# Kernel optimization log

Hardware: AMD Instinct MI355X
Metric: run time of the kernel (lower is better)

The kernel has to match this reference:

```python
import jax, jax.numpy as jnp
import numpy as np

B, C, N = 16, 128, 16384


def setup_inputs() -> dict:
    key = jax.random.key(0)
    k1, k2, k3, k4, k5 = jax.random.split(key, 5)
    scale = 1.0 / np.sqrt(C)
    return {
        "feature": jax.random.normal(k1, (B, C, N), dtype=jnp.float32),
        "position": jax.random.normal(k2, (B, C, N), dtype=jnp.float32),
        "Wq": jax.random.normal(k3, (C, C), dtype=jnp.float32) * scale,
        "Wk": jax.random.normal(k4, (C, C), dtype=jnp.float32) * scale,
        "Wv": jax.random.normal(k5, (C, C), dtype=jnp.float32) * scale,
    }


def reference(feature, position, Wq, Wk, Wv):
    # 1x1 Conv1d == channel-mixing matmul: (B,C,N) x (Cout,Cin) -> (B,Cout,N)
    q = jnp.einsum("oc,bcn->bon", Wq, position)  # (B,C,N)
    k = jnp.einsum("oc,bcn->bon", Wk, position)  # (B,C,N)
    v = jnp.einsum("oc,bcn->bon", Wv, feature)   # (B,C,N)

    # torch: matmul((B,N,C,1),(B,N,1,C)).sum(dim=-2) == (sum_c q) * k
    # -> energy[b,j,n] = sq[b,n] * k[b,j,n], avoiding the (B,N,C,C) tensor.
    sq = jnp.sum(q, axis=1, keepdims=True)       # (B,1,N)
    energy = sq * k                              # (B,C,N)

    # normalize over the channel axis (torch's dim=-1 on (B,N,C) layout)
    energy = energy / (1e-9 + jnp.sum(energy, axis=1, keepdims=True))

    # softmax over channel axis (torch: Softmax(dim=1) on permuted (B,C,N))
    attention = jax.nn.softmax(energy, axis=1)   # (B,C,N)

    return attention * v + feature               # (B,C,N)
```

## Files before the change

### kernel.cpp

```cpp
#include <hip/hip_runtime.h>

#define B_ 16
#define C_ 128
#define N_ 16384
#define TN 32

typedef __attribute__((ext_vector_type(8))) short short8;
typedef __attribute__((ext_vector_type(4))) float f32x4;

__device__ inline unsigned short bf16_rn(float x) {
  unsigned u = __float_as_uint(x);
  unsigned r = u + 0x7FFFu + ((u >> 16) & 1u);
  return (unsigned short)(r >> 16);
}

__device__ inline unsigned cvt_pk_bf16(float a, float b) {
  unsigned r;
  asm("v_cvt_pk_bf16_f32 %0, %1, %2" : "=v"(r) : "v"(a), "v"(b));
  return r;
}

__global__ __launch_bounds__(256) void prep_kernel(
    const float* __restrict__ Wq, const float* __restrict__ Wk, const float* __restrict__ Wv,
    float* __restrict__ wqsum,
    unsigned short* __restrict__ WkHi, unsigned short* __restrict__ WkLo,
    unsigned short* __restrict__ WvHi) {
  int idx = blockIdx.x * 256 + threadIdx.x;
  {
    float x = Wk[idx];
    unsigned short h = bf16_rn(x);
    WkHi[idx] = h;
    WkLo[idx] = bf16_rn(x - __uint_as_float(((unsigned)h) << 16));
  }
  WvHi[idx] = bf16_rn(Wv[idx]);
  if (blockIdx.x == 0 && threadIdx.x < C_) {
    int i = threadIdx.x;
    float s = 0.f;
#pragma unroll 8
    for (int o = 0; o < C_; ++o) s += Wq[o * C_ + i];
    wqsum[i] = s;
  }
}

__global__ __launch_bounds__(256, 6) void csa_mfma_kernel(
    const float* __restrict__ feature, const float* __restrict__ position,
    const float* __restrict__ wqsum,
    const unsigned short* __restrict__ WkHi, const unsigned short* __restrict__ WkLo,
    const unsigned short* __restrict__ WvHi,
    float* __restrict__ out) {
  __shared__ unsigned short posHi[TN * 128];
  __shared__ unsigned short posLo[TN * 128];
  __shared__ unsigned short featHi[TN * 128];
  __shared__ float red0[4][TN];
  __shared__ float red1[4][TN];
  __shared__ float red2[4][TN];
  __shared__ float red3[4][TN];

  const int tid = threadIdx.x;
  const int lane = tid & 63;
  const int w = tid >> 6;
  const int m = lane & 15;
  const int q = lane >> 4;
  const int b = blockIdx.x >> 9;
  const int n0 = (blockIdx.x & 511) * TN;

  const float* pos_g = position + (size_t)b * C_ * N_ + n0;
  const float* feat_g = feature + (size_t)b * C_ * N_ + n0;

  {
    const int g = tid >> 3;
    const int n4 = (tid & 7) * 4;
    f32x4 sqa = (f32x4){0.f, 0.f, 0.f, 0.f};
#pragma unroll
    for (int it = 0; it < 2; ++it) {
      int i = 64 * it + 2 * g;
      float4 p0 = *(const float4*)(pos_g + (size_t)i * N_ + n4);
      float4 p1 = *(const float4*)(pos_g + (size_t)(i + 1) * N_ + n4);
      float4 f0 = *(const float4*)(feat_g + (size_t)i * N_ + n4);
      float4 f1 = *(const float4*)(feat_g + (size_t)(i + 1) * N_ + n4);
      float2 wq2 = *(const float2*)(wqsum + i);
      const float* P0 = (const float*)&p0;
      const float* P1 = (const float*)&p1;
      const float* F0 = (const float*)&f0;
      const float* F1 = (const float*)&f1;
      int c8 = (i >> 3) * 8;
      int ioff = i & 7;
#pragma unroll
      for (int d = 0; d < 4; ++d) {
        int n = n4 + d;
        int fn8 = ((n & 15) ^ ((n >> 2) & 7)) * 8;
        int hw = n * 128 + (c8 ^ fn8) + ioff;
        float x0 = P0[d], x1 = P1[d];
        unsigned hu = cvt_pk_bf16(x0, x1);
        *(unsigned*)(posHi + hw) = hu;
        float l0 = x0 - __uint_as_float(hu << 16);
        float l1 = x1 - __uint_as_float(hu & 0xFFFF0000u);
        *(unsigned*)(posLo + hw) = cvt_pk_bf16(l0, l1);
        *(unsigned*)(featHi + hw) = cvt_pk_bf16(F0[d], F1[d]);
        sqa[d] = fmaf(wq2.x, x0, fmaf(wq2.y, x1, sqa[d]));
      }
    }
#pragma unroll
    for (int d = 0; d < 4; ++d) {
      float s = sqa[d];
      s += __shfl_xor(s, 8, 64);
      s += __shfl_xor(s, 16, 64);
      s += __shfl_xor(s, 32, 64);
      sqa[d] = s;
    }
    if (lane < 8) {
      *(float4*)&red0[w][lane * 4] =
          make_float4(sqa[0], sqa[1], sqa[2], sqa[3]);
    }
  }
  __syncthreads();

  int rb[2], f8[2];
#pragma unroll
  for (int nt = 0; nt < 2; ++nt) {
    int n = nt * 16 + m;
    rb[nt] = n * 128;
    f8[nt] = ((n & 15) ^ ((n >> 2) & 7)) * 8;
  }

  f32x4 acck[2][2];
#pragma unroll
  for (int jt = 0; jt < 2; ++jt)
#pragma unroll
    for (int nt = 0; nt < 2; ++nt) acck[jt][nt] = (f32x4){0.f, 0.f, 0.f, 0.f};

#pragma unroll
  for (int jt = 0; jt < 2; ++jt) {
    const int arow = (32 * w + 16 * jt + m) * 128 + q * 8;
    short8 ah[4], al[4];
#pragma unroll
    for (int kk = 0; kk < 4; ++kk) {
      ah[kk] = *(const short8*)(WkHi + arow + kk * 32);
      al[kk] = *(const short8*)(WkLo + arow + kk * 32);
    }
#pragma unroll
    for (int kk = 0; kk < 4; ++kk) {
      int co = (kk * 4 + q) * 8;
      short8 bh0 = *(const short8*)(posHi + rb[0] + (co ^ f8[0]));
      short8 bl0 = *(const short8*)(posLo + rb[0] + (co ^ f8[0]));
      short8 bh1 = *(const short8*)(posHi + rb[1] + (co ^ f8[1]));
      short8 bl1 = *(const short8*)(posLo + rb[1] + (co ^ f8[1]));
      acck[jt][0] = __builtin_amdgcn_mfma_f32_16x16x32_bf16(ah[kk], bh0, acck[jt][0], 0, 0, 0);
      acck[jt][1] = __builtin_amdgcn_mfma_f32_16x16x32_bf16(ah[kk], bh1, acck[jt][1], 0, 0, 0);
      acck[jt][0] = __builtin_amdgcn_mfma_f32_16x16x32_bf16(ah[kk], bl0, acck[jt][0], 0, 0, 0);
      acck[jt][1] = __builtin_amdgcn_mfma_f32_16x16x32_bf16(ah[kk], bl1, acck[jt][1], 0, 0, 0);
      acck[jt][0] = __builtin_amdgcn_mfma_f32_16x16x32_bf16(al[kk], bh0, acck[jt][0], 0, 0, 0);
      acck[jt][1] = __builtin_amdgcn_mfma_f32_16x16x32_bf16(al[kk], bh1, acck[jt][1], 0, 0, 0);
    }
  }

#pragma unroll
  for (int nt = 0; nt < 2; ++nt) {
    float s = 0.f;
#pragma unroll
    for (int jt = 0; jt < 2; ++jt)
      s += acck[jt][nt][0] + acck[jt][nt][1] + acck[jt][nt][2] + acck[jt][nt][3];
    s += __shfl_xor(s, 16, 64);
    s += __shfl_xor(s, 32, 64);
    if (q == 0) red1[w][nt * 16 + m] = s;
  }

  f32x4 accv[2][2];
#pragma unroll
  for (int jt = 0; jt < 2; ++jt)
#pragma unroll
    for (int nt = 0; nt < 2; ++nt) accv[jt][nt] = (f32x4){0.f, 0.f, 0.f, 0.f};

#pragma unroll
  for (int jt = 0; jt < 2; ++jt) {
    const int arow = (32 * w + 16 * jt + m) * 128 + q * 8;
    short8 ah[4];
#pragma unroll
    for (int kk = 0; kk < 4; ++kk) ah[kk] = *(const short8*)(WvHi + arow + kk * 32);
#pragma unroll
    for (int kk = 0; kk < 4; ++kk) {
      int co = (kk * 4 + q) * 8;
      short8 bh0 = *(const short8*)(featHi + rb[0] + (co ^ f8[0]));
      short8 bh1 = *(const short8*)(featHi + rb[1] + (co ^ f8[1]));
      accv[jt][0] = __builtin_amdgcn_mfma_f32_16x16x32_bf16(ah[kk], bh0, accv[jt][0], 0, 0, 0);
      accv[jt][1] = __builtin_amdgcn_mfma_f32_16x16x32_bf16(ah[kk], bh1, accv[jt][1], 0, 0, 0);
    }
  }
  __syncthreads();

  float mw[2], sw[2], attscale[2];
#pragma unroll
  for (int nt = 0; nt < 2; ++nt) {
    int c = nt * 16 + m;
    float ss = red0[0][c] + red0[1][c] + red0[2][c] + red0[3][c];
    float ks = red1[0][c] + red1[1][c] + red1[2][c] + red1[3][c];
    float gl = (ss / (1e-9f + ss * ks)) * 1.44269504f;
    float mx = gl * acck[0][nt][0];
#pragma unroll
    for (int jt = 0; jt < 2; ++jt)
#pragma unroll
      for (int r = 0; r < 4; ++r) {
        float e = gl * acck[jt][nt][r];
        acck[jt][nt][r] = e;
        mx = fmaxf(mx, e);
      }
    mx = fmaxf(mx, __shfl_xor(mx, 16, 64));
    mx = fmaxf(mx, __shfl_xor(mx, 32, 64));
    float s = 0.f;
#pragma unroll
    for (int jt = 0; jt < 2; ++jt)
#pragma unroll
      for (int r = 0; r < 4; ++r) {
        float p = exp2f(acck[jt][nt][r] - mx);
        acck[jt][nt][r] = p;
        s += p;
      }
    s += __shfl_xor(s, 16, 64);
    s += __shfl_xor(s, 32, 64);
    mw[nt] = mx;
    sw[nt] = s;
  }
  if (q == 0) {
#pragma unroll
    for (int nt = 0; nt < 2; ++nt) {
      red2[w][nt * 16 + m] = mw[nt];
      red3[w][nt * 16 + m] = sw[nt];
    }
  }
  __syncthreads();
#pragma unroll
  for (int nt = 0; nt < 2; ++nt) {
    int c = nt * 16 + m;
    float M = red2[0][c];
    M = fmaxf(M, red2[1][c]);
    M = fmaxf(M, red2[2][c]);
    M = fmaxf(M, red2[3][c]);
    float es = red3[0][c] * exp2f(red2[0][c] - M);
    es += red3[1][c] * exp2f(red2[1][c] - M);
    es += red3[2][c] * exp2f(red2[2][c] - M);
    es += red3[3][c] * exp2f(red2[3][c] - M);
    attscale[nt] = exp2f(mw[nt] - M) / es;
  }

  float* outp = out + (size_t)b * C_ * N_ + n0 + m;
  const float* finp = feature + (size_t)b * C_ * N_ + n0 + m;
#pragma unroll
  for (int jt = 0; jt < 2; ++jt) {
    const int jb = 32 * w + 16 * jt + 4 * q;
#pragma unroll
    for (int nt = 0; nt < 2; ++nt) {
      float as = attscale[nt];
      size_t base = (size_t)jb * N_ + nt * 16;
      float fv0 = finp[base];
      float fv1 = finp[base + N_];
      float fv2 = finp[base + (size_t)2 * N_];
      float fv3 = finp[base + (size_t)3 * N_];
      outp[base] = fmaf(acck[jt][nt][0] * as, accv[jt][nt][0], fv0);
      outp[base + N_] = fmaf(acck[jt][nt][1] * as, accv[jt][nt][1], fv1);
      outp[base + (size_t)2 * N_] = fmaf(acck[jt][nt][2] * as, accv[jt][nt][2], fv2);
      outp[base + (size_t)3 * N_] = fmaf(acck[jt][nt][3] * as, accv[jt][nt][3], fv3);
    }
  }
}

extern "C" void kernel_launch(void* const* d_in, const int* in_sizes, int n_in,
                              void* d_out, int out_size, void* d_ws, size_t ws_size,
                              hipStream_t stream) {
  const float* feature = (const float*)d_in[0];
  const float* position = (const float*)d_in[1];
  const float* Wq = (const float*)d_in[2];
  const float* Wk = (const float*)d_in[3];
  const float* Wv = (const float*)d_in[4];
  float* out = (float*)d_out;

  char* ws = (char*)d_ws;
  float* wqsum = (float*)ws;
  unsigned short* WkHi = (unsigned short*)(ws + 512);
  unsigned short* WkLo = (unsigned short*)(ws + 512 + 32768);
  unsigned short* WvHi = (unsigned short*)(ws + 512 + 65536);

  prep_kernel<<<64, 256, 0, stream>>>(Wq, Wk, Wv, wqsum, WkHi, WkLo, WvHi);
  csa_mfma_kernel<<<B_ * (N_ / TN), 256, 0, stream>>>(feature, position, wqsum,
                                                      WkHi, WkLo, WvHi, out);
}
```

Baseline: 399.0 us.

## Process multiple tiles per block with register prefetch and LDS-based residual

Each block now handles four consecutive 32-column tiles, issuing global loads for the next tile into registers while computing the current one. Feature is also split into hi/lo bf16 in LDS so the residual add reconstructs it from shared memory instead of re-reading global memory. This aims to hide load latency and cut redundant DRAM traffic, at the cost of fewer blocks, higher register/LDS use, lower occupancy, and slightly reduced precision of the residual term.

Result: slower. 519.5 us (+30.2%).

```diff
diff --git a/kernel.cpp b/kernel.cpp
--- a/kernel.cpp
+++ b/kernel.cpp
@@ -4,6 +4,7 @@
 #define C_ 128
 #define N_ 16384
 #define TN 32
+#define NT 4
 
 typedef __attribute__((ext_vector_type(8))) short short8;
 typedef __attribute__((ext_vector_type(4))) float f32x4;
@@ -19,6 +20,9 @@
   asm("v_cvt_pk_bf16_f32 %0, %1, %2" : "=v"(r) : "v"(a), "v"(b));
   return r;
 }
+
+__device__ inline float u16hi_f(unsigned u) { return __uint_as_float(u & 0xFFFF0000u); }
+__device__ inline float u16lo_f(unsigned u) { return __uint_as_float(u << 16); }
 
 __global__ __launch_bounds__(256) void prep_kernel(
     const float* __restrict__ Wq, const float* __restrict__ Wk, const float* __restrict__ Wv,
@@ -42,7 +46,7 @@
   }
 }
 
-__global__ __launch_bounds__(256, 6) void csa_mfma_kernel(
+__global__ __launch_bounds__(256, 4) void csa_mfma_kernel(
     const float* __restrict__ feature, const float* __restrict__ position,
     const float* __restrict__ wqsum,
     const unsigned short* __restrict__ WkHi, const unsigned short* __restrict__ WkLo,
@@ -51,6 +55,7 @@
   __shared__ unsigned short posHi[TN * 128];
   __shared__ unsigned short posLo[TN * 128];
   __shared__ unsigned short featHi[TN * 128];
+  __shared__ unsigned short featLo[TN * 128];
   __shared__ float red0[4][TN];
   __shared__ float red1[4][TN];
   __shared__ float red2[4][TN];
@@ -61,28 +66,50 @@
   const int w = tid >> 6;
   const int m = lane & 15;
   const int q = lane >> 4;
-  const int b = blockIdx.x >> 9;
-  const int n0 = (blockIdx.x & 511) * TN;
-
-  const float* pos_g = position + (size_t)b * C_ * N_ + n0;
-  const float* feat_g = feature + (size_t)b * C_ * N_ + n0;
-
-  {
-    const int g = tid >> 3;
-    const int n4 = (tid & 7) * 4;
-    f32x4 sqa = (f32x4){0.f, 0.f, 0.f, 0.f};
+  const int b = blockIdx.x >> 7;
+  const int ncol0 = (blockIdx.x & 127) * (TN * NT);
+
+  const float* pos_g = position + (size_t)b * C_ * N_ + ncol0;
+  const float* feat_g = feature + (size_t)b * C_ * N_ + ncol0;
+
+  const int g = tid >> 3;
+  const int n4 = (tid & 7) * 4;
+  const float2 wq0 = *(const float2*)(wqsum + 2 * g);
+  const float2 wq1 = *(const float2*)(wqsum + 64 + 2 * g);
+
+  int rb[2], f8[2];
+#pragma unroll
+  for (int nt = 0; nt < 2; ++nt) {
+    int n = nt * 16 + m;
+    rb[nt] = n * 128;
+    f8[nt] = ((n & 15) ^ ((n >> 2) & 7)) * 8;
+  }
+
+  float4 P0[2], P1[2], F0[2], F1[2];
+
+  auto issue_loads = [&](int t) {
+    const float* pg = pos_g + t * TN;
+    const float* fg = feat_g + t * TN;
 #pragma unroll
     for (int it = 0; it < 2; ++it) {
       int i = 64 * it + 2 * g;
-      float4 p0 = *(const float4*)(pos_g + (size_t)i * N_ + n4);
-      float4 p1 = *(const float4*)(pos_g + (size_t)(i + 1) * N_ + n4);
-      float4 f0 = *(const float4*)(feat_g + (size_t)i * N_ + n4);
-      float4 f1 = *(const float4*)(feat_g + (size_t)(i + 1) * N_ + n4);
-      float2 wq2 = *(const float2*)(wqsum + i);
-      const float* P0 = (const float*)&p0;
-      const float* P1 = (const float*)&p1;
-      const float* F0 = (const float*)&f0;
-      const float* F1 = (const float*)&f1;
+      P0[it] = *(const float4*)(pg + (size_t)i * N_ + n4);
+      P1[it] = *(const float4*)(pg + (size_t)(i + 1) * N_ + n4);
+      F0[it] = *(const float4*)(fg + (size_t)i * N_ + n4);
+      F1[it] = *(const float4*)(fg + (size_t)(i + 1) * N_ + n4);
+    }
+  };
+
+  auto stage_convert = [&]() {
+    f32x4 sqa = (f32x4){0.f, 0.f, 0.f, 0.f};
+#pragma unroll
+    for (int it = 0; it < 2; ++it) {
+      int i = 64 * it + 2 * g;
+      float2 wq2 = it ? wq1 : wq0;
+      const float* P0p = (const float*)&P0[it];
+      const float* P1p = (const float*)&P1[it];
+      const float* F0p = (const float*)&F0[it];
+      const float* F1p = (const float*)&F1[it];
       int c8 = (i >> 3) * 8;
       int ioff = i & 7;
 #pragma unroll
@@ -90,13 +117,18 @@
         int n = n4 + d;
         int fn8 = ((n & 15) ^ ((n >> 2) & 7)) * 8;
         int hw = n * 128 + (c8 ^ fn8) + ioff;
-        float x0 = P0[d], x1 = P1[d];
+        float x0 = P0p[d], x1 = P1p[d];
         unsigned hu = cvt_pk_bf16(x0, x1);
         *(unsigned*)(posHi + hw) = hu;
-        float l0 = x0 - __uint_as_float(hu << 16);
-        float l1 = x1 - __uint_as_float(hu & 0xFFFF0000u);
+        float l0 = x0 - u16lo_f(hu);
+        float l1 = x1 - u16hi_f(hu);
         *(unsigned*)(posLo + hw) = cvt_pk_bf16(l0, l1);
-        *(unsigned*)(featHi + hw) = cvt_pk_bf16(F0[d], F1[d]);
+        float y0 = F0p[d], y1 = F1p[d];
+        unsigned fu = cvt_pk_bf16(y0, y1);
+        *(unsigned*)(featHi + hw) = fu;
+        float e0 = y0 - u16lo_f(fu);
+        float e1 = y1 - u16hi_f(fu);
+        *(unsigned*)(featLo + hw) = cvt_pk_bf16(e0, e1);
         sqa[d] = fmaf(wq2.x, x0, fmaf(wq2.y, x1, sqa[d]));
       }
     }
@@ -109,156 +141,176 @@
       sqa[d] = s;
     }
     if (lane < 8) {
-      *(float4*)&red0[w][lane * 4] =
-          make_float4(sqa[0], sqa[1], sqa[2], sqa[3]);
-    }
-  }
+      *(float4*)&red0[w][lane * 4] = make_float4(sqa[0], sqa[1], sqa[2], sqa[3]);
+    }
+  };
+
+  issue_loads(0);
+  stage_convert();
   __syncthreads();
 
-  int rb[2], f8[2];
-#pragma unroll
-  for (int nt = 0; nt < 2; ++nt) {
-    int n = nt * 16 + m;
-    rb[nt] = n * 128;
-    f8[nt] = ((n & 15) ^ ((n >> 2) & 7)) * 8;
-  }
-
-  f32x4 acck[2][2];
-#pragma unroll
-  for (int jt = 0; jt < 2; ++jt)
-#pragma unroll
-    for (int nt = 0; nt < 2; ++nt) acck[jt][nt] = (f32x4){0.f, 0.f, 0.f, 0.f};
-
-#pragma unroll
-  for (int jt = 0; jt < 2; ++jt) {
-    const int arow = (32 * w + 16 * jt + m) * 128 + q * 8;
-    short8 ah[4], al[4];
-#pragma unroll
-    for (int kk = 0; kk < 4; ++kk) {
-      ah[kk] = *(const short8*)(WkHi + arow + kk * 32);
-      al[kk] = *(const short8*)(WkLo + arow + kk * 32);
-    }
-#pragma unroll
-    for (int kk = 0; kk < 4; ++kk) {
-      int co = (kk * 4 + q) * 8;
-      short8 bh0 = *(const short8*)(posHi + rb[0] + (co ^ f8[0]));
-      short8 bl0 = *(const short8*)(posLo + rb[0] + (co ^ f8[0]));
-      short8 bh1 = *(const short8*)(posHi + rb[1] + (co ^ f8[1]));
-      short8 bl1 = *(const short8*)(posLo + rb[1] + (co ^ f8[1]));
-      acck[jt][0] = __builtin_amdgcn_mfma_f32_16x16x32_bf16(ah[kk], bh0, acck[jt][0], 0, 0, 0);
-      acck[jt][1] = __builtin_amdgcn_mfma_f32_16x16x32_bf16(ah[kk], bh1, acck[jt][1], 0, 0, 0);
-      acck[jt][0] = __builtin_amdgcn_mfma_f32_16x16x32_bf16(ah[kk], bl0, acck[jt][0], 0, 0, 0);
-      acck[jt][1] = __builtin_amdgcn_mfma_f32_16x16x32_bf16(ah[kk], bl1, acck[jt][1], 0, 0, 0);
-      acck[jt][0] = __builtin_amdgcn_mfma_f32_16x16x32_bf16(al[kk], bh0, acck[jt][0], 0, 0, 0);
-      acck[jt][1] = __builtin_amdgcn_mfma_f32_16x16x32_bf16(al[kk], bh1, acck[jt][1], 0, 0, 0);
-    }
-  }
-
-#pragma unroll
-  for (int nt = 0; nt < 2; ++nt) {
-    float s = 0.f;
+#pragma unroll
+  for (int t = 0; t < NT; ++t) {
+    if (t + 1 < NT) issue_loads(t + 1);
+
+    f32x4 acck[2][2];
 #pragma unroll
     for (int jt = 0; jt < 2; ++jt)
-      s += acck[jt][nt][0] + acck[jt][nt][1] + acck[jt][nt][2] + acck[jt][nt][3];
-    s += __shfl_xor(s, 16, 64);
-    s += __shfl_xor(s, 32, 64);
-    if (q == 0) red1[w][nt * 16 + m] = s;
-  }
-
-  f32x4 accv[2][2];
-#pragma unroll
-  for (int jt = 0; jt < 2; ++jt)
-#pragma unroll
-    for (int nt = 0; nt < 2; ++nt) accv[jt][nt] = (f32x4){0.f, 0.f, 0.f, 0.f};
-
-#pragma unroll
-  for (int jt = 0; jt < 2; ++jt) {
-    const int arow = (32 * w + 16 * jt + m) * 128 + q * 8;
-    short8 ah[4];
-#pragma unroll
-    for (int kk = 0; kk < 4; ++kk) ah[kk] = *(const short8*)(WvHi + arow + kk * 32);
-#pragma unroll
-    for (int kk = 0; kk < 4; ++kk) {
-      int co = (kk * 4 + q) * 8;
-      short8 bh0 = *(const short8*)(featHi + rb[0] + (co ^ f8[0]));
-      short8 bh1 = *(const short8*)(featHi + rb[1] + (co ^ f8[1]));
-      accv[jt][0] = __builtin_amdgcn_mfma_f32_16x16x32_bf16(ah[kk], bh0, accv[jt][0], 0, 0, 0);
-      accv[jt][1] = __builtin_amdgcn_mfma_f32_16x16x32_bf16(ah[kk], bh1, accv[jt][1], 0, 0, 0);
-    }
-  }
-  __syncthreads();
-
-  float mw[2], sw[2], attscale[2];
-#pragma unroll
-  for (int nt = 0; nt < 2; ++nt) {
-    int c = nt * 16 + m;
-    float ss = red0[0][c] + red0[1][c] + red0[2][c] + red0[3][c];
-    float ks = red1[0][c] + red1[1][c] + red1[2][c] + red1[3][c];
-    float gl = (ss / (1e-9f + ss * ks)) * 1.44269504f;
-    float mx = gl * acck[0][nt][0];
+#pragma unroll
+      for (int nt = 0; nt < 2; ++nt) acck[jt][nt] = (f32x4){0.f, 0.f, 0.f, 0.f};
+
+#pragma unroll
+    for (int jt = 0; jt < 2; ++jt) {
+      const int arow = (32 * w + 16 * jt + m) * 128 + q * 8;
+      short8 ah[4], al[4];
+#pragma unroll
+      for (int kk = 0; kk < 4; ++kk) {
+        ah[kk] = *(const short8*)(WkHi + arow + kk * 32);
+        al[kk] = *(const short8*)(WkLo + arow + kk * 32);
+      }
+#pragma unroll
+      for (int kk = 0; kk < 4; ++kk) {
+        int co = (kk * 4 + q) * 8;
+        short8 bh0 = *(const short8*)(posHi + rb[0] + (co ^ f8[0]));
+        short8 bl0 = *(const short8*)(posLo + rb[0] + (co ^ f8[0]));
+        short8 bh1 = *(const short8*)(posHi + rb[1] + (co ^ f8[1]));
+        short8 bl1 = *(const short8*)(posLo + rb[1] + (co ^ f8[1]));
+        acck[jt][0] = __builtin_amdgcn_mfma_f32_16x16x32_bf16(ah[kk], bh0, acck[jt][0], 0, 0, 0);
+        acck[jt][1] = __builtin_amdgcn_mfma_f32_16x16x32_bf16(ah[kk], bh1, acck[jt][1], 0, 0, 0);
+        acck[jt][0] = __builtin_amdgcn_mfma_f32_16x16x32_bf16(ah[kk], bl0, acck[jt][0], 0, 0, 0);
+        acck[jt][1] = __builtin_amdgcn_mfma_f32_16x16x32_bf16(ah[kk], bl1, acck[jt][1], 0, 0, 0);
+        acck[jt][0] = __builtin_amdgcn_mfma_f32_16x16x32_bf16(al[kk], bh0, acck[jt][0], 0, 0, 0);
+        acck[jt][1] = __builtin_amdgcn_mfma_f32_16x16x32_bf16(al[kk], bh1, acck[jt][1], 0, 0, 0);
+      }
+    }
+
+#pragma unroll
+    for (int nt = 0; nt < 2; ++nt) {
+      float s = 0.f;
+#pragma unroll
+      for (int jt = 0; jt < 2; ++jt)
+        s += acck[jt][nt][0] + acck[jt][nt][1] + acck[jt][nt][2] + acck[jt][nt][3];
+      s += __shfl_xor(s, 16, 64);
+      s += __shfl_xor(s, 32, 64);
+      if (q == 0) red1[w][nt * 16 + m] = s;
+    }
+
+    f32x4 accv[2][2];
 #pragma unroll
     for (int jt = 0; jt < 2; ++jt)
 #pragma unroll
-      for (int r = 0; r < 4; ++r) {
-        float e = gl * acck[jt][nt][r];
-        acck[jt][nt][r] = e;
-        mx = fmaxf(mx, e);
-      }
-    mx = fmaxf(mx, __shfl_xor(mx, 16, 64));
-    mx = fmaxf(mx, __shfl_xor(mx, 32, 64));
-    float s = 0.f;
-#pragma unroll
-    for (int jt = 0; jt < 2; ++jt)
-#pragma unroll
-      for (int r = 0; r < 4; ++r) {
-        float p = exp2f(acck[jt][nt][r] - mx);
-        acck[jt][nt][r] = p;
-        s += p;
-      }
-    s += __shfl_xor(s, 16, 64);
-    s += __shfl_xor(s, 32, 64);
-    mw[nt] = mx;
-    sw[nt] = s;
-  }
-  if (q == 0) {
+      for (int nt = 0; nt < 2; ++nt) accv[jt][nt] = (f32x4){0.f, 0.f, 0.f, 0.f};
+
+#pragma unroll
+    for (int jt = 0; jt < 2; ++jt) {
+      const int arow = (32 * w + 16 * jt + m) * 128 + q * 8;
+      short8 ah[4];
+#pragma unroll
+      for (int kk = 0; kk < 4; ++kk) ah[kk] = *(const short8*)(WvHi + arow + kk * 32);
+#pragma unroll
+      for (int kk = 0; kk < 4; ++kk) {
+        int co = (kk * 4 + q) * 8;
+        short8 bh0 = *(const short8*)(featHi + rb[0] + (co ^ f8[0]));
+        short8 bh1 = *(const short8*)(featHi + rb[1] + (co ^ f8[1]));
+        accv[jt][0] = __builtin_amdgcn_mfma_f32_16x16x32_bf16(ah[kk], bh0, accv[jt][0], 0, 0, 0);
+        accv[jt][1] = __builtin_amdgcn_mfma_f32_16x16x32_bf16(ah[kk], bh1, accv[jt][1], 0, 0, 0);
+      }
+    }
+
+    float fv[2][2][4];
+#pragma unroll
+    for (int jt = 0; jt < 2; ++jt) {
+      const int jb = 32 * w + 16 * jt + 4 * q;
+      const int cj = (jb >> 3) * 8;
+      const int joff = jb & 7;
+#pragma unroll
+      for (int nt = 0; nt < 2; ++nt) {
+        int hw = rb[nt] + (cj ^ f8[nt]) + joff;
+        unsigned fh01 = *(const unsigned*)(featHi + hw);
+        unsigned fl01 = *(const unsigned*)(featLo + hw);
+        unsigned fh23 = *(const unsigned*)(featHi + hw + 2);
+        unsigned fl23 = *(const unsigned*)(featLo + hw + 2);
+        fv[jt][nt][0] = u16lo_f(fh01) + u16lo_f(fl01);
+        fv[jt][nt][1] = u16hi_f(fh01) + u16hi_f(fl01);
+        fv[jt][nt][2] = u16lo_f(fh23) + u16lo_f(fl23);
+        fv[jt][nt][3] = u16hi_f(fh23) + u16hi_f(fl23);
+      }
+    }
+
+    __syncthreads();
+
+    float mw[2], sw[2], attscale[2];
 #pragma unroll
     for (int nt = 0; nt < 2; ++nt) {
-      red2[w][nt * 16 + m] = mw[nt];
-      red3[w][nt * 16 + m] = sw[nt];
-    }
-  }
-  __syncthreads();
-#pragma unroll
-  for (int nt = 0; nt < 2; ++nt) {
-    int c = nt * 16 + m;
-    float M = red2[0][c];
-    M = fmaxf(M, red2[1][c]);
-    M = fmaxf(M, red2[2][c]);
-    M = fmaxf(M, red2[3][c]);
-    float es = red3[0][c] * exp2f(red2[0][c] - M);
-    es += red3[1][c] * exp2f(red2[1][c] - M);
-    es += red3[2][c] * exp2f(red2[2][c] - M);
-    es += red3[3][c] * exp2f(red2[3][c] - M);
-    attscale[nt] = exp2f(mw[nt] - M) / es;
-  }
-
-  float* outp = out + (size_t)b * C_ * N_ + n0 + m;
-  const float* finp = feature + (size_t)b * C_ * N_ + n0 + m;
-#pragma unroll
-  for (int jt = 0; jt < 2; ++jt) {
-    const int jb = 32 * w + 16 * jt + 4 * q;
+      int c = nt * 16 + m;
+      float ss = red0[0][c] + red0[1][c] + red0[2][c] + red0[3][c];
+      float ks = red1[0][c] + red1[1][c] + red1[2][c] + red1[3][c];
+      float gl = (ss / (1e-9f + ss * ks)) * 1.44269504f;
+      float mx = gl * acck[0][nt][0];
+#pragma unroll
+      for (int jt = 0; jt < 2; ++jt)
+#pragma unroll
+        for (int r = 0; r < 4; ++r) {
+          float e = gl * acck[jt][nt][r];
+          acck[jt][nt][r] = e;
+          mx = fmaxf(mx, e);
+        }
+      mx = fmaxf(mx, __shfl_xor(mx, 16, 64));
+      mx = fmaxf(mx, __shfl_xor(mx, 32, 64));
+      float s = 0.f;
+#pragma unroll
+      for (int jt = 0; jt < 2; ++jt)
+#pragma unroll
+        for (int r = 0; r < 4; ++r) {
+          float p = exp2f(acck[jt][nt][r] - mx);
+          acck[jt][nt][r] = p;
+          s += p;
+        }
+      s += __shfl_xor(s, 16, 64);
+      s += __shfl_xor(s, 32, 64);
+      mw[nt] = mx;
+      sw[nt] = s;
+    }
+    if (q == 0) {
+#pragma unroll
+      for (int nt = 0; nt < 2; ++nt) {
+        red2[w][nt * 16 + m] = mw[nt];
+        red3[w][nt * 16 + m] = sw[nt];
+      }
+    }
+    __syncthreads();
 #pragma unroll
     for (int nt = 0; nt < 2; ++nt) {
-      float as = attscale[nt];
-      size_t base = (size_t)jb * N_ + nt * 16;
-      float fv0 = finp[base];
-      float fv1 = finp[base + N_];
-      float fv2 = finp[base + (size_t)2 * N_];
-      float fv3 = finp[base + (size_t)3 * N_];
-      outp[base] = fmaf(acck[jt][nt][0] * as, accv[jt][nt][0], fv0);
-      outp[base + N_] = fmaf(acck[jt][nt][1] * as, accv[jt][nt][1], fv1);
-      outp[base + (size_t)2 * N_] = fmaf(acck[jt][nt][2] * as, accv[jt][nt][2], fv2);
-      outp[base + (size_t)3 * N_] = fmaf(acck[jt][nt][3] * as, accv[jt][nt][3], fv3);
+      int c = nt * 16 + m;
+      float M = red2[0][c];
+      M = fmaxf(M, red2[1][c]);
+      M = fmaxf(M, red2[2][c]);
+      M = fmaxf(M, red2[3][c]);
+      float es = red3[0][c] * exp2f(red2[0][c] - M);
+      es += red3[1][c] * exp2f(red2[1][c] - M);
+      es += red3[2][c] * exp2f(red2[2][c] - M);
+      es += red3[3][c] * exp2f(red2[3][c] - M);
+      attscale[nt] = exp2f(mw[nt] - M) / es;
+    }
+
+    float* outp = out + (size_t)b * C_ * N_ + ncol0 + t * TN + m;
+#pragma unroll
+    for (int jt = 0; jt < 2; ++jt) {
+      const int jb = 32 * w + 16 * jt + 4 * q;
+#pragma unroll
+      for (int nt = 0; nt < 2; ++nt) {
+        float as = attscale[nt];
+        size_t base = (size_t)jb * N_ + nt * 16;
+        outp[base] = fmaf(acck[jt][nt][0] * as, accv[jt][nt][0], fv[jt][nt][0]);
+        outp[base + N_] = fmaf(acck[jt][nt][1] * as, accv[jt][nt][1], fv[jt][nt][1]);
+        outp[base + (size_t)2 * N_] = fmaf(acck[jt][nt][2] * as, accv[jt][nt][2], fv[jt][nt][2]);
+        outp[base + (size_t)3 * N_] = fmaf(acck[jt][nt][3] * as, accv[jt][nt][3], fv[jt][nt][3]);
+      }
+    }
+
+    if (t + 1 < NT) {
+      stage_convert();
+      __syncthreads();
     }
   }
 }
@@ -280,6 +332,6 @@
   unsigned short* WvHi = (unsigned short*)(ws + 512 + 65536);
 
   prep_kernel<<<64, 256, 0, stream>>>(Wq, Wk, Wv, wqsum, WkHi, WkLo, WvHi);
-  csa_mfma_kernel<<<B_ * (N_ / TN), 256, 0, stream>>>(feature, position, wqsum,
-                                                      WkHi, WkLo, WvHi, out);
-}
+  csa_mfma_kernel<<<B_ * (N_ / (TN * NT)), 256, 0, stream>>>(feature, position, wqsum,
+                                                             WkHi, WkLo, WvHi, out);
+}
```

## Reuse LDS tiles for feature and rebuild residual from hi/lo bf16 split

Applied to the files above, without the earlier changes.

Position and feature now share two LDS tiles: position is staged first for the K projection, then feature is loaded into the same buffers after the softmax statistics. The residual feature values are reconstructed from the hi+lo bf16 pair in LDS instead of being re-read from global memory. The smaller LDS footprint allows the launch bound to rise to 8 blocks per CU. The cost is an extra barrier-serialised phase for the feature load and a slight precision loss in the residual term.

Measured after the change: 436.1 us. +9.3%, slower.

```diff
diff --git a/kernel.cpp b/kernel.cpp
--- a/kernel.cpp
+++ b/kernel.cpp
@@ -19,6 +19,9 @@
   asm("v_cvt_pk_bf16_f32 %0, %1, %2" : "=v"(r) : "v"(a), "v"(b));
   return r;
 }
+
+__device__ inline float u16hi_f(unsigned u) { return __uint_as_float(u & 0xFFFF0000u); }
+__device__ inline float u16lo_f(unsigned u) { return __uint_as_float(u << 16); }
 
 __global__ __launch_bounds__(256) void prep_kernel(
     const float* __restrict__ Wq, const float* __restrict__ Wk, const float* __restrict__ Wv,
@@ -42,15 +45,14 @@
   }
 }
 
-__global__ __launch_bounds__(256, 6) void csa_mfma_kernel(
+__global__ __launch_bounds__(256, 8) void csa_mfma_kernel(
     const float* __restrict__ feature, const float* __restrict__ position,
     const float* __restrict__ wqsum,
     const unsigned short* __restrict__ WkHi, const unsigned short* __restrict__ WkLo,
     const unsigned short* __restrict__ WvHi,
     float* __restrict__ out) {
-  __shared__ unsigned short posHi[TN * 128];
-  __shared__ unsigned short posLo[TN * 128];
-  __shared__ unsigned short featHi[TN * 128];
+  __shared__ unsigned short xHi[TN * 128];
+  __shared__ unsigned short xLo[TN * 128];
   __shared__ float red0[4][TN];
   __shared__ float red1[4][TN];
   __shared__ float red2[4][TN];
@@ -67,22 +69,27 @@
   const float* pos_g = position + (size_t)b * C_ * N_ + n0;
   const float* feat_g = feature + (size_t)b * C_ * N_ + n0;
 
+  const int g = tid >> 3;
+  const int n4 = (tid & 7) * 4;
+
+  int rb[2], f8[2];
+#pragma unroll
+  for (int nt = 0; nt < 2; ++nt) {
+    int n = nt * 16 + m;
+    rb[nt] = n * 128;
+    f8[nt] = ((n & 15) ^ ((n >> 2) & 7)) * 8;
+  }
+
   {
-    const int g = tid >> 3;
-    const int n4 = (tid & 7) * 4;
     f32x4 sqa = (f32x4){0.f, 0.f, 0.f, 0.f};
 #pragma unroll
     for (int it = 0; it < 2; ++it) {
       int i = 64 * it + 2 * g;
       float4 p0 = *(const float4*)(pos_g + (size_t)i * N_ + n4);
       float4 p1 = *(const float4*)(pos_g + (size_t)(i + 1) * N_ + n4);
-      float4 f0 = *(const float4*)(feat_g + (size_t)i * N_ + n4);
-      float4 f1 = *(const float4*)(feat_g + (size_t)(i + 1) * N_ + n4);
       float2 wq2 = *(const float2*)(wqsum + i);
       const float* P0 = (const float*)&p0;
       const float* P1 = (const float*)&p1;
-      const float* F0 = (const float*)&f0;
-      const float* F1 = (const float*)&f1;
       int c8 = (i >> 3) * 8;
       int ioff = i & 7;
 #pragma unroll
@@ -92,11 +99,10 @@
         int hw = n * 128 + (c8 ^ fn8) + ioff;
         float x0 = P0[d], x1 = P1[d];
         unsigned hu = cvt_pk_bf16(x0, x1);
-        *(unsigned*)(posHi + hw) = hu;
-        float l0 = x0 - __uint_as_float(hu << 16);
-        float l1 = x1 - __uint_as_float(hu & 0xFFFF0000u);
-        *(unsigned*)(posLo + hw) = cvt_pk_bf16(l0, l1);
-        *(unsigned*)(featHi + hw) = cvt_pk_bf16(F0[d], F1[d]);
+        *(unsigned*)(xHi + hw) = hu;
+        float l0 = x0 - u16lo_f(hu);
+        float l1 = x1 - u16hi_f(hu);
+        *(unsigned*)(xLo + hw) = cvt_pk_bf16(l0, l1);
         sqa[d] = fmaf(wq2.x, x0, fmaf(wq2.y, x1, sqa[d]));
       }
     }
@@ -109,19 +115,10 @@
       sqa[d] = s;
     }
     if (lane < 8) {
-      *(float4*)&red0[w][lane * 4] =
-          make_float4(sqa[0], sqa[1], sqa[2], sqa[3]);
+      *(float4*)&red0[w][lane * 4] = make_float4(sqa[0], sqa[1], sqa[2], sqa[3]);
     }
   }
   __syncthreads();
-
-  int rb[2], f8[2];
-#pragma unroll
-  for (int nt = 0; nt < 2; ++nt) {
-    int n = nt * 16 + m;
-    rb[nt] = n * 128;
-    f8[nt] = ((n & 15) ^ ((n >> 2) & 7)) * 8;
-  }
 
   f32x4 acck[2][2];
 #pragma unroll
@@ -141,10 +138,10 @@
 #pragma unroll
     for (int kk = 0; kk < 4; ++kk) {
       int co = (kk * 4 + q) * 8;
-      short8 bh0 = *(const short8*)(posHi + rb[0] + (co ^ f8[0]));
-      short8 bl0 = *(const short8*)(posLo + rb[0] + (co ^ f8[0]));
-      short8 bh1 = *(const short8*)(posHi + rb[1] + (co ^ f8[1]));
-      short8 bl1 = *(const short8*)(posLo + rb[1] + (co ^ f8[1]));
+      short8 bh0 = *(const short8*)(xHi + rb[0] + (co ^ f8[0]));
+      short8 bl0 = *(const short8*)(xLo + rb[0] + (co ^ f8[0]));
+      short8 bh1 = *(const short8*)(xHi + rb[1] + (co ^ f8[1]));
+      short8 bl1 = *(const short8*)(xLo + rb[1] + (co ^ f8[1]));
       acck[jt][0] = __builtin_amdgcn_mfma_f32_16x16x32_bf16(ah[kk], bh0, acck[jt][0], 0, 0, 0);
       acck[jt][1] = __builtin_amdgcn_mfma_f32_16x16x32_bf16(ah[kk], bh1, acck[jt][1], 0, 0, 0);
       acck[jt][0] = __builtin_amdgcn_mfma_f32_16x16x32_bf16(ah[kk], bl0, acck[jt][0], 0, 0, 0);
@@ -164,31 +161,9 @@
     s += __shfl_xor(s, 32, 64);
     if (q == 0) red1[w][nt * 16 + m] = s;
   }
-
-  f32x4 accv[2][2];
-#pragma unroll
-  for (int jt = 0; jt < 2; ++jt)
-#pragma unroll
-    for (int nt = 0; nt < 2; ++nt) accv[jt][nt] = (f32x4){0.f, 0.f, 0.f, 0.f};
-
-#pragma unroll
-  for (int jt = 0; jt < 2; ++jt) {
-    const int arow = (32 * w + 16 * jt + m) * 128 + q * 8;
-    short8 ah[4];
-#pragma unroll
-    for (int kk = 0; kk < 4; ++kk) ah[kk] = *(const short8*)(WvHi + arow + kk * 32);
-#pragma unroll
-    for (int kk = 0; kk < 4; ++kk) {
-      int co = (kk * 4 + q) * 8;
-      short8 bh0 = *(const short8*)(featHi + rb[0] + (co ^ f8[0]));
-      short8 bh1 = *(const short8*)(featHi + rb[1] + (co ^ f8[1]));
-      accv[jt][0] = __builtin_amdgcn_mfma_f32_16x16x32_bf16(ah[kk], bh0, accv[jt][0], 0, 0, 0);
-      accv[jt][1] = __builtin_amdgcn_mfma_f32_16x16x32_bf16(ah[kk], bh1, accv[jt][1], 0, 0, 0);
-    }
-  }
   __syncthreads();
 
-  float mw[2], sw[2], attscale[2];
+  float mw[2], sw[2];
 #pragma unroll
   for (int nt = 0; nt < 2; ++nt) {
     int c = nt * 16 + m;
@@ -227,7 +202,34 @@
       red3[w][nt * 16 + m] = sw[nt];
     }
   }
+
+  {
+#pragma unroll
+    for (int it = 0; it < 2; ++it) {
+      int i = 64 * it + 2 * g;
+      float4 f0 = *(const float4*)(feat_g + (size_t)i * N_ + n4);
+      float4 f1 = *(const float4*)(feat_g + (size_t)(i + 1) * N_ + n4);
+      const float* F0 = (const float*)&f0;
+      const float* F1 = (const float*)&f1;
+      int c8 = (i >> 3) * 8;
+      int ioff = i & 7;
+#pragma unroll
+      for (int d = 0; d < 4; ++d) {
+        int n = n4 + d;
+        int fn8 = ((n & 15) ^ ((n >> 2) & 7)) * 8;
+        int hw = n * 128 + (c8 ^ fn8) + ioff;
+        float y0 = F0[d], y1 = F1[d];
+        unsigned fu = cvt_pk_bf16(y0, y1);
+        *(unsigned*)(xHi + hw) = fu;
+        float e0 = y0 - u16lo_f(fu);
+        float e1 = y1 - u16hi_f(fu);
+        *(unsigned*)(xLo + hw) = cvt_pk_bf16(e0, e1);
+      }
+    }
+  }
   __syncthreads();
+
+  float attscale[2];
 #pragma unroll
   for (int nt = 0; nt < 2; ++nt) {
     int c = nt * 16 + m;
@@ -242,19 +244,47 @@
     attscale[nt] = exp2f(mw[nt] - M) / es;
   }
 
+  f32x4 accv[2][2];
+#pragma unroll
+  for (int jt = 0; jt < 2; ++jt)
+#pragma unroll
+    for (int nt = 0; nt < 2; ++nt) accv[jt][nt] = (f32x4){0.f, 0.f, 0.f, 0.f};
+
+#pragma unroll
+  for (int jt = 0; jt < 2; ++jt) {
+    const int arow = (32 * w + 16 * jt + m) * 128 + q * 8;
+    short8 ah[4];
+#pragma unroll
+    for (int kk = 0; kk < 4; ++kk) ah[kk] = *(const short8*)(WvHi + arow + kk * 32);
+#pragma unroll
+    for (int kk = 0; kk < 4; ++kk) {
+      int co = (kk * 4 + q) * 8;
+      short8 bh0 = *(const short8*)(xHi + rb[0] + (co ^ f8[0]));
+      short8 bh1 = *(const short8*)(xHi + rb[1] + (co ^ f8[1]));
+      accv[jt][0] = __builtin_amdgcn_mfma_f32_16x16x32_bf16(ah[kk], bh0, accv[jt][0], 0, 0, 0);
+      accv[jt][1] = __builtin_amdgcn_mfma_f32_16x16x32_bf16(ah[kk], bh1, accv[jt][1], 0, 0, 0);
+    }
+  }
+
   float* outp = out + (size_t)b * C_ * N_ + n0 + m;
-  const float* finp = feature + (size_t)b * C_ * N_ + n0 + m;
 #pragma unroll
   for (int jt = 0; jt < 2; ++jt) {
     const int jb = 32 * w + 16 * jt + 4 * q;
+    const int cj = (jb >> 3) * 8;
+    const int joff = jb & 7;
 #pragma unroll
     for (int nt = 0; nt < 2; ++nt) {
+      int hw = rb[nt] + (cj ^ f8[nt]) + joff;
+      unsigned fh01 = *(const unsigned*)(xHi + hw);
+      unsigned fl01 = *(const unsigned*)(xLo + hw);
+      unsigned fh23 = *(const unsigned*)(xHi + hw + 2);
+      unsigned fl23 = *(const unsigned*)(xLo + hw + 2);
+      float fv0 = u16lo_f(fh01) + u16lo_f(fl01);
+      float fv1 = u16hi_f(fh01) + u16hi_f(fl01);
+      float fv2 = u16lo_f(fh23) + u16lo_f(fl23);
+      float fv3 = u16hi_f(fh23) + u16hi_f(fl23);
       float as = attscale[nt];
       size_t base = (size_t)jb * N_ + nt * 16;
-      float fv0 = finp[base];
-      float fv1 = finp[base + N_];
-      float fv2 = finp[base + (size_t)2 * N_];
-      float fv3 = finp[base + (size_t)3 * N_];
       outp[base] = fmaf(acck[jt][nt][0] * as, accv[jt][nt][0], fv0);
       outp[base + N_] = fmaf(acck[jt][nt][1] * as, accv[jt][nt][1], fv1);
       outp[base + (size_t)2 * N_] = fmaf(acck[jt][nt][2] * as, accv[jt][nt][2], fv2);
```
